# Kernel tuning notes

Measured on AMD Instinct MI355X. Metric: run time of the kernel, lower is better.

## Reference

```python
import jax, jax.numpy as jnp
import numpy as np

B, T, C, NH = 4, 2048, 1024, 16
HS = C // NH  # 64


def setup_inputs() -> dict:
    key = jax.random.key(0)
    ks = jax.random.split(key, 3)
    x = jax.random.normal(ks[0], (B, T, C), dtype=jnp.float32)
    w_attn = jax.random.normal(ks[1], (C, 3 * C), dtype=jnp.float32) * (1.0 / np.sqrt(C))
    b_attn = jnp.zeros((3 * C,), dtype=jnp.float32)
    w_proj = jax.random.normal(ks[2], (C, C), dtype=jnp.float32) * (1.0 / np.sqrt(C))
    b_proj = jnp.zeros((C,), dtype=jnp.float32)
    return {"x": x, "w_attn": w_attn, "b_attn": b_attn, "w_proj": w_proj, "b_proj": b_proj}


def reference(x, w_attn, b_attn, w_proj, b_proj):
    Bx, Tx, Cx = x.shape
    qkv = x @ w_attn + b_attn                      # (B,T,3C)
    q, k, v = jnp.split(qkv, 3, axis=2)
    # faithful to torch: view(B,T,hs,nh).transpose(1,3) -> (B,nh,hs,T)
    def to_heads(t):
        return jnp.transpose(t.reshape(Bx, Tx, HS, NH), (0, 3, 2, 1))
    q, k, v = to_heads(q), to_heads(k), to_heads(v)
    # att[b,h,i,j] = q_i . k_j / sqrt(hs)
    att = jnp.einsum('bhdi,bhdj->bhij', q, k) * (1.0 / np.sqrt(HS))
    # buffer is tril.T == upper-triangular; keep i<=j, mask i>j
    keep = jnp.triu(jnp.ones((Tx, Tx), dtype=bool))[None, None]
    att = jnp.where(keep, att, -jnp.inf)
    att = jax.nn.softmax(att, axis=-2)             # normalize over i
    y = jnp.einsum('bhdi,bhij->bhdj', v, att)      # (B,nh,hs,T)
    y = jnp.transpose(y, (0, 3, 2, 1)).reshape(Bx, Tx, Cx)
    return y @ w_proj + b_proj
```

## Files before the change

kernel.cpp:

```cpp
#include <hip/hip_runtime.h>
#include <stdint.h>


typedef __attribute__((ext_vector_type(8))) _Float16 f16x8;
typedef __attribute__((ext_vector_type(4))) _Float16 f16x4;
typedef __attribute__((ext_vector_type(2))) _Float16 h2;
typedef __attribute__((ext_vector_type(2))) __fp16   fp16x2_t;
typedef __attribute__((ext_vector_type(4))) float    f32x4;

#define NT_   8192
#define NC_   1024
#define N3C_  3072

__device__ __forceinline__ uint32_t pkrtz(float a, float b){
  union { fp16x2_t h; uint32_t u; } cv;
  cv.h = __builtin_amdgcn_cvt_pkrtz(a, b);
  return cv.u;
}

__global__ void k_cvt(const float* __restrict__ src, _Float16* __restrict__ dst, int n4){
  int idx = blockIdx.x*blockDim.x + threadIdx.x;
  int stride = gridDim.x*blockDim.x;
  for (int i = idx; i < n4; i += stride){
    float4 v = ((const float4*)src)[i];
    f16x4 o;
    o[0] = (_Float16)v.x; o[1] = (_Float16)v.y;
    o[2] = (_Float16)v.z; o[3] = (_Float16)v.w;
    ((f16x4*)dst)[i] = o;
  }
}

__global__ void k_wattn_t(const float* __restrict__ w, _Float16* __restrict__ wt){
  int t = threadIdx.x;
  int m0 = blockIdx.x*128, c0 = blockIdx.y*32;
  int mcol = m0 + t;
  int part = mcol >> 10, rr = mcol & 1023;
  int mp = part*1024 + (rr & 15)*64 + (rr >> 4);
  alignas(16) _Float16 buf[32];
  #pragma unroll
  for (int cc = 0; cc < 32; cc++)
    buf[cc] = (_Float16)w[(size_t)(c0+cc)*N3C_ + mcol];
  uint4* dst = (uint4*)(wt + (size_t)mp*NC_ + c0);
  const uint4* sb = (const uint4*)buf;
  dst[0]=sb[0]; dst[1]=sb[1]; dst[2]=sb[2]; dst[3]=sb[3];
}

__global__ void k_wproj_t(const float* __restrict__ w, _Float16* __restrict__ wt){
  int t = threadIdx.x;
  int o0 = blockIdx.x*128, cp0 = blockIdx.y*32;
  int o = o0 + t;
  alignas(16) _Float16 buf[32];
  #pragma unroll
  for (int i = 0; i < 32; i++){
    int cp = cp0 + i;
    int row = (cp & 63)*16 + (cp >> 6);
    buf[i] = (_Float16)w[(size_t)row*NC_ + o];
  }
  uint4* dst = (uint4*)(wt + (size_t)o*NC_ + cp0);
  const uint4* sb = (const uint4*)buf;
  dst[0]=sb[0]; dst[1]=sb[1]; dst[2]=sb[2]; dst[3]=sb[3];
}

__global__ void k_bias(const float* __restrict__ ba, float* __restrict__ bp){
  int i = blockIdx.x*blockDim.x + threadIdx.x;
  int part = i >> 10, rr = i & 1023, h = rr >> 6, d = rr & 63;
  bp[i] = ba[part*1024 + d*16 + h];
}

template<int OUT_HALF>
__global__ __launch_bounds__(256) void k_gemm(
    const _Float16* __restrict__ A, const _Float16* __restrict__ BT,
    const float* __restrict__ bias, void* __restrict__ outp,
    _Float16* __restrict__ VTout,
    int M, int N, int K)
{
  __shared__ _Float16 As[128][40];
  __shared__ _Float16 Bs[128][40];
  int tid = threadIdx.x;
  int wave = tid >> 6, lane = tid & 63;
  int wr = wave >> 1, wc = wave & 1;
  int g = lane >> 4, l15 = lane & 15;
  f32x4 acc[4][4] = {};
  const _Float16* Ag = A  + (size_t)blockIdx.y*128*K;
  const _Float16* Bg = BT + (size_t)blockIdx.x*128*K;
  int srow = tid >> 1, skoff = (tid & 1)*16;
  const _Float16* apt = Ag + (size_t)srow*K + skoff;
  const _Float16* bpt = Bg + (size_t)srow*K + skoff;
  uint4 ra0 = *(const uint4*)apt;
  uint4 ra1 = *(const uint4*)(apt + 8);
  uint4 rb0 = *(const uint4*)bpt;
  uint4 rb1 = *(const uint4*)(bpt + 8);
  for (int kt = 0; kt < K; kt += 32){
    __syncthreads();
    *(uint4*)&As[srow][skoff]     = ra0;
    *(uint4*)&As[srow][skoff + 8] = ra1;
    *(uint4*)&Bs[srow][skoff]     = rb0;
    *(uint4*)&Bs[srow][skoff + 8] = rb1;
    __syncthreads();
    if (kt + 32 < K){
      ra0 = *(const uint4*)(apt + kt + 32);
      ra1 = *(const uint4*)(apt + kt + 40);
      rb0 = *(const uint4*)(bpt + kt + 32);
      rb1 = *(const uint4*)(bpt + kt + 40);
    }
    f16x8 af[4], bf[4];
    #pragma unroll
    for (int mi = 0; mi < 4; mi++) af[mi] = *(const f16x8*)&As[wr*64 + mi*16 + l15][g*8];
    #pragma unroll
    for (int ni = 0; ni < 4; ni++) bf[ni] = *(const f16x8*)&Bs[wc*64 + ni*16 + l15][g*8];
    #pragma unroll
    for (int mi = 0; mi < 4; mi++)
      #pragma unroll
      for (int ni = 0; ni < 4; ni++)
        acc[mi][ni] = __builtin_amdgcn_mfma_f32_16x16x32_f16(af[mi], bf[ni], acc[mi][ni], 0, 0, 0);
  }
  int rowBase = blockIdx.y*128 + wr*64;
  int colBase = blockIdx.x*128 + wc*64;
  if (OUT_HALF && colBase >= 2048){
    int b = rowBase >> 11;
    int t0 = (rowBase & 2047);
    #pragma unroll
    for (int mi = 0; mi < 4; mi++){
      #pragma unroll
      for (int ni = 0; ni < 4; ni++){
        int col = colBase + ni*16 + l15;
        int cc = col - 2048;
        int h = cc >> 6, d = cc & 63;
        float bv = bias[col];
        _Float16* dst = VTout + (((size_t)(b*16 + h)*64 + d)*2048) + t0 + mi*16 + g*4;
        f16x4 o;
        #pragma unroll
        for (int r = 0; r < 4; r++) o[r] = (_Float16)(acc[mi][ni][r] + bv);
        *(f16x4*)dst = o;
      }
    }
    return;
  }
  #pragma unroll
  for (int mi = 0; mi < 4; mi++){
    #pragma unroll
    for (int ni = 0; ni < 4; ni++){
      int col = colBase + ni*16 + l15;
      float bv = bias[col];
      #pragma unroll
      for (int r = 0; r < 4; r++){
        int row = rowBase + mi*16 + g*4 + r;
        float v = acc[mi][ni][r] + bv;
        if (OUT_HALF) ((_Float16*)outp)[(size_t)row*N + col] = (_Float16)v;
        else          ((float*)outp)[(size_t)row*N + col] = v;
      }
    }
  }
}

__global__ __launch_bounds__(256) void k_attn(
    const _Float16* __restrict__ qkv, const _Float16* __restrict__ VTb,
    _Float16* __restrict__ Y)
{
  __shared__ _Float16 Ks[2][64][64];
  __shared__ _Float16 Vs[2][64][64];
  __shared__ uint32_t Ps[4][16][32];
  int bid = blockIdx.x;
  int bh = bid & 63;
  int j = bid >> 6;
  const int jts[4] = { j, 15-j, 16+j, 31-j };
  int maxjt = 31 - j;
  int b = bh >> 4, h = bh & 15;
  int tid = threadIdx.x, wave = tid >> 6, lane = tid & 63;
  int g = lane >> 4, l15 = lane & 15;
  uint32_t* Pw = &Ps[wave][0][0] + l15*32;
  int xm = (l15 & 7) << 2;
  int swR = (l15 & 7) << 4;
  const _Float16 QS = (_Float16)0.18033688f;
  const float OFF = 12.0f;

  int q0[4];
  f16x8 qf0[4], qf1[4];
  #pragma unroll
  for (int t = 0; t < 4; t++){
    q0[t] = jts[t]*64 + wave*16;
    const _Float16* qp = qkv + (size_t)(b*2048 + q0[t] + l15)*N3C_ + 1024 + h*64;
    qf0[t] = *(const f16x8*)&qp[g*8] * QS;
    qf1[t] = *(const f16x8*)&qp[32 + g*8] * QS;
  }
  float lrun[4] = {0.f, 0.f, 0.f, 0.f};
  f32x4 acc[4][4] = {};

  int srow = tid >> 2;
  int sbyte = (tid & 3)*32;
  int swW = (srow & 7) << 4;
  const _Float16* kbase = qkv + (size_t)(b*2048 + srow)*N3C_ + h*64 + (sbyte>>1);
  const _Float16* vbase = VTb + ((size_t)bh*64 + srow)*2048 + (sbyte>>1);

  auto stage = [&](int buf, const uint4& k0, const uint4& k1,
                   const uint4& v0, const uint4& v1){
    char* kw = (char*)&Ks[buf][0][0] + srow*128;
    char* vw = (char*)&Vs[buf][0][0] + srow*128;
    *(uint4*)(kw + ( sbyte       ^ swW)) = k0;
    *(uint4*)(kw + ((sbyte + 16) ^ swW)) = k1;
    *(uint4*)(vw + ( sbyte       ^ swW)) = v0;
    *(uint4*)(vw + ((sbyte + 16) ^ swW)) = v1;
  };

  auto process = [&](const f16x8& qa, const f16x8& qb, float& lr,
                     f32x4* ac, int qt0, int i0, bool diag, int cur){
    const char* kb = (const char*)&Ks[cur][0][0];
    const char* vb = (const char*)&Vs[cur][0][0];
    f32x4 s2[4];
    #pragma unroll
    for (int nb = 0; nb < 4; nb++){
      const char* krow = kb + (nb*16 + l15)*128;
      f16x8 kf0 = *(const f16x8*)(krow + (( g*16)      ^ swR));
      f16x8 kf1 = *(const f16x8*)(krow + ((64 + g*16)  ^ swR));
      f32x4 z = {};
      z = __builtin_amdgcn_mfma_f32_16x16x32_f16(kf0, qa, z, 0, 0, 0);
      z = __builtin_amdgcn_mfma_f32_16x16x32_f16(kf1, qb, z, 0, 0, 0);
      s2[nb] = z;
    }
    float p[16];
    #pragma unroll
    for (int nb = 0; nb < 4; nb++)
      #pragma unroll
      for (int r = 0; r < 4; r++)
        p[nb*4 + r] = s2[nb][r];
    if (diag){
      int qidx = qt0 + l15;
      #pragma unroll
      for (int nb = 0; nb < 4; nb++)
        #pragma unroll
        for (int r = 0; r < 4; r++){
          int kidx = i0 + nb*16 + g*4 + r;
          if (kidx > qidx) p[nb*4 + r] = -3e30f;
        }
    }
    uint32_t pk[8];
    #pragma unroll
    for (int i = 0; i < 8; i++){
      float e0 = __builtin_amdgcn_exp2f(p[2*i]     - OFF);
      float e1 = __builtin_amdgcn_exp2f(p[2*i + 1] - OFF);
      pk[i] = pkrtz(e0, e1);
    }
    #pragma unroll
    for (int nb = 0; nb < 4; nb++)
      #pragma unroll
      for (int r2 = 0; r2 < 2; r2++)
        Pw[(nb*8 + g*2 + r2) ^ xm] = pk[nb*2 + r2];
    #pragma unroll
    for (int ks = 0; ks < 2; ks++){
      f16x8 pb = *(const f16x8*)&Pw[(ks*16 + g*4) ^ xm];
      #pragma unroll
      for (int db = 0; db < 4; db++){
        const char* vrow = vb + (db*16 + l15)*128;
        f16x8 vv = *(const f16x8*)(vrow + ((ks*64 + g*16) ^ swR));
        ac[db] = __builtin_amdgcn_mfma_f32_16x16x32_f16(vv, pb, ac[db], 0, 0, 0);
      }
    }
    const h2 ones = { (_Float16)1.0f, (_Float16)1.0f };
    union { uint32_t u; h2 h; } cv;
    float rs0 = 0.f, rs1 = 0.f;
    #pragma unroll
    for (int i = 0; i < 4; i++){
      cv.u = pk[i];     rs0 = __builtin_amdgcn_fdot2(cv.h, ones, rs0, false);
      cv.u = pk[i + 4]; rs1 = __builtin_amdgcn_fdot2(cv.h, ones, rs1, false);
    }
    lr += rs0 + rs1;
  };

  uint4 ka0 = *(const uint4*)&kbase[0];
  uint4 ka1 = *(const uint4*)&kbase[8];
  uint4 va0 = *(const uint4*)&vbase[0];
  uint4 va1 = *(const uint4*)&vbase[8];
  stage(0, ka0, ka1, va0, va1);
  __syncthreads();
  for (int it = 0; it <= maxjt; ++it){
    int cur = it & 1;
    if (it < maxjt){
      size_t ko = (size_t)(it+1)*64*N3C_;
      int    vo = (it+1)*64;
      ka0 = *(const uint4*)&kbase[ko];
      ka1 = *(const uint4*)&kbase[ko + 8];
      va0 = *(const uint4*)&vbase[vo];
      va1 = *(const uint4*)&vbase[vo + 8];
    }
    #pragma unroll
    for (int t = 0; t < 4; t++)
      if (it <= jts[t])
        process(qf0[t], qf1[t], lrun[t], acc[t], q0[t], it*64, it == jts[t], cur);
    if (it < maxjt) stage(cur ^ 1, ka0, ka1, va0, va1);
    __syncthreads();
  }

  #pragma unroll
  for (int t = 0; t < 4; t++){
    float rs = lrun[t];
    rs += __shfl_xor(rs, 16);
    rs += __shfl_xor(rs, 32);
    float inv = 1.0f / rs;
    _Float16* yb = Y + (size_t)(b*2048 + q0[t] + l15)*NC_ + h*64 + g*4;
    #pragma unroll
    for (int db = 0; db < 4; db++){
      f16x4 o;
      #pragma unroll
      for (int r = 0; r < 4; r++) o[r] = (_Float16)(acc[t][db][r]*inv);
      *(f16x4*)&yb[db*16] = o;
    }
  }
}

extern "C" void kernel_launch(void* const* d_in, const int* in_sizes, int n_in,
                              void* d_out, int out_size, void* d_ws, size_t ws_size,
                              hipStream_t stream)
{
  const float* x      = (const float*)d_in[0];
  const float* w_attn = (const float*)d_in[1];
  const float* b_attn = (const float*)d_in[2];
  const float* w_proj = (const float*)d_in[3];
  const float* b_proj = (const float*)d_in[4];
  float* out = (float*)d_out;
  char* ws = (char*)d_ws;
  _Float16* xb   = (_Float16*)(ws + 0);
  _Float16* wT   = (_Float16*)(ws + 16777216);
  _Float16* wpT  = (_Float16*)(ws + 23068672);
  float*    bp   = (float*)   (ws + 25165824);
  _Float16* qkv  = (_Float16*)(ws + 25178112);
  _Float16* VT   = (_Float16*)(ws + 75509760);
  _Float16* Y    = (_Float16*)(ws + 92286976);

  k_cvt<<<2048, 256, 0, stream>>>(x, xb, (NT_*NC_)/4);
  k_wattn_t<<<dim3(24, 32), 128, 0, stream>>>(w_attn, wT);
  k_wproj_t<<<dim3(8, 32), 128, 0, stream>>>(w_proj, wpT);
  k_bias<<<12, 256, 0, stream>>>(b_attn, bp);
  k_gemm<1><<<dim3(24, 64), 256, 0, stream>>>(xb, wT, bp, qkv, VT, NT_, N3C_, NC_);
  k_attn<<<512, 256, 0, stream>>>(qkv, VT, Y);
  k_gemm<0><<<dim3(8, 64), 256, 0, stream>>>(Y, wpT, b_proj, out, (_Float16*)nullptr, NT_, NC_, NC_);
}
```

Baseline: 197.5 us.

## Double GEMM K-tile and attention KV tile to cut barrier and staging overhead

The GEMM now stages 64-wide K slices per iteration instead of 32, with wider LDS rows and two MFMA sub-steps per tile. This halves the number of global-to-LDS round trips and barriers. The attention kernel processes 128 keys per iteration instead of 64, again halving loop iterations and syncs. In exchange, LDS use rises (about 80KB for attention), which can lower occupancy, and some diagonal tiles now compute a fully masked 64-key half.

```diff
diff --git a/kernel.cpp b/kernel.cpp
--- a/kernel.cpp
+++ b/kernel.cpp
@@ -74,8 +74,8 @@
     _Float16* __restrict__ VTout,
     int M, int N, int K)
 {
-  __shared__ _Float16 As[128][40];
-  __shared__ _Float16 Bs[128][40];
+  __shared__ _Float16 As[128][72];
+  __shared__ _Float16 Bs[128][72];
   int tid = threadIdx.x;
   int wave = tid >> 6, lane = tid & 63;
   int wr = wave >> 1, wc = wave & 1;
@@ -83,36 +83,43 @@
   f32x4 acc[4][4] = {};
   const _Float16* Ag = A  + (size_t)blockIdx.y*128*K;
   const _Float16* Bg = BT + (size_t)blockIdx.x*128*K;
-  int srow = tid >> 1, skoff = (tid & 1)*16;
+  int srow = tid >> 1, skoff = (tid & 1)*32;
   const _Float16* apt = Ag + (size_t)srow*K + skoff;
   const _Float16* bpt = Bg + (size_t)srow*K + skoff;
-  uint4 ra0 = *(const uint4*)apt;
-  uint4 ra1 = *(const uint4*)(apt + 8);
-  uint4 rb0 = *(const uint4*)bpt;
-  uint4 rb1 = *(const uint4*)(bpt + 8);
-  for (int kt = 0; kt < K; kt += 32){
+  uint4 ra[4], rb[4];
+  #pragma unroll
+  for (int i = 0; i < 4; i++){
+    ra[i] = *(const uint4*)(apt + i*8);
+    rb[i] = *(const uint4*)(bpt + i*8);
+  }
+  for (int kt = 0; kt < K; kt += 64){
     __syncthreads();
-    *(uint4*)&As[srow][skoff]     = ra0;
-    *(uint4*)&As[srow][skoff + 8] = ra1;
-    *(uint4*)&Bs[srow][skoff]     = rb0;
-    *(uint4*)&Bs[srow][skoff + 8] = rb1;
+    #pragma unroll
+    for (int i = 0; i < 4; i++){
+      *(uint4*)&As[srow][skoff + i*8] = ra[i];
+      *(uint4*)&Bs[srow][skoff + i*8] = rb[i];
+    }
     __syncthreads();
-    if (kt + 32 < K){
-      ra0 = *(const uint4*)(apt + kt + 32);
-      ra1 = *(const uint4*)(apt + kt + 40);
-      rb0 = *(const uint4*)(bpt + kt + 32);
-      rb1 = *(const uint4*)(bpt + kt + 40);
-    }
-    f16x8 af[4], bf[4];
-    #pragma unroll
-    for (int mi = 0; mi < 4; mi++) af[mi] = *(const f16x8*)&As[wr*64 + mi*16 + l15][g*8];
-    #pragma unroll
-    for (int ni = 0; ni < 4; ni++) bf[ni] = *(const f16x8*)&Bs[wc*64 + ni*16 + l15][g*8];
-    #pragma unroll
-    for (int mi = 0; mi < 4; mi++)
-      #pragma unroll
-      for (int ni = 0; ni < 4; ni++)
-        acc[mi][ni] = __builtin_amdgcn_mfma_f32_16x16x32_f16(af[mi], bf[ni], acc[mi][ni], 0, 0, 0);
+    if (kt + 64 < K){
+      #pragma unroll
+      for (int i = 0; i < 4; i++){
+        ra[i] = *(const uint4*)(apt + kt + 64 + i*8);
+        rb[i] = *(const uint4*)(bpt + kt + 64 + i*8);
+      }
+    }
+    #pragma unroll
+    for (int kk = 0; kk < 2; kk++){
+      f16x8 af[4], bf[4];
+      #pragma unroll
+      for (int mi = 0; mi < 4; mi++) af[mi] = *(const f16x8*)&As[wr*64 + mi*16 + l15][kk*32 + g*8];
+      #pragma unroll
+      for (int ni = 0; ni < 4; ni++) bf[ni] = *(const f16x8*)&Bs[wc*64 + ni*16 + l15][kk*32 + g*8];
+      #pragma unroll
+      for (int mi = 0; mi < 4; mi++)
+        #pragma unroll
+        for (int ni = 0; ni < 4; ni++)
+          acc[mi][ni] = __builtin_amdgcn_mfma_f32_16x16x32_f16(af[mi], bf[ni], acc[mi][ni], 0, 0, 0);
+    }
   }
   int rowBase = blockIdx.y*128 + wr*64;
   int colBase = blockIdx.x*128 + wc*64;
@@ -157,28 +164,28 @@
     const _Float16* __restrict__ qkv, const _Float16* __restrict__ VTb,
     _Float16* __restrict__ Y)
 {
-  __shared__ _Float16 Ks[2][64][64];
-  __shared__ _Float16 Vs[2][64][64];
-  __shared__ uint32_t Ps[4][16][32];
+  __shared__ _Float16 Ks[2][128][64];
+  __shared__ _Float16 Vs[2][64][128];
+  __shared__ uint32_t Ps[4][16][64];
   int bid = blockIdx.x;
   int bh = bid & 63;
   int j = bid >> 6;
   const int jts[4] = { j, 15-j, 16+j, 31-j };
-  int maxjt = 31 - j;
   int b = bh >> 4, h = bh & 15;
   int tid = threadIdx.x, wave = tid >> 6, lane = tid & 63;
   int g = lane >> 4, l15 = lane & 15;
-  uint32_t* Pw = &Ps[wave][0][0] + l15*32;
+  uint32_t* Pw = &Ps[wave][0][0] + l15*64;
   int xm = (l15 & 7) << 2;
   int swR = (l15 & 7) << 4;
   const _Float16 QS = (_Float16)0.18033688f;
   const float OFF = 12.0f;
 
-  int q0[4];
+  int q0[4], lastt[4];
   f16x8 qf0[4], qf1[4];
   #pragma unroll
   for (int t = 0; t < 4; t++){
     q0[t] = jts[t]*64 + wave*16;
+    lastt[t] = jts[t] >> 1;
     const _Float16* qp = qkv + (size_t)(b*2048 + q0[t] + l15)*N3C_ + 1024 + h*64;
     qf0[t] = *(const f16x8*)&qp[g*8] * QS;
     qf1[t] = *(const f16x8*)&qp[32 + g*8] * QS;
@@ -186,72 +193,70 @@
   float lrun[4] = {0.f, 0.f, 0.f, 0.f};
   f32x4 acc[4][4] = {};
 
-  int srow = tid >> 2;
-  int sbyte = (tid & 3)*32;
-  int swW = (srow & 7) << 4;
-  const _Float16* kbase = qkv + (size_t)(b*2048 + srow)*N3C_ + h*64 + (sbyte>>1);
-  const _Float16* vbase = VTb + ((size_t)bh*64 + srow)*2048 + (sbyte>>1);
-
-  auto stage = [&](int buf, const uint4& k0, const uint4& k1,
-                   const uint4& v0, const uint4& v1){
-    char* kw = (char*)&Ks[buf][0][0] + srow*128;
-    char* vw = (char*)&Vs[buf][0][0] + srow*128;
-    *(uint4*)(kw + ( sbyte       ^ swW)) = k0;
-    *(uint4*)(kw + ((sbyte + 16) ^ swW)) = k1;
-    *(uint4*)(vw + ( sbyte       ^ swW)) = v0;
-    *(uint4*)(vw + ((sbyte + 16) ^ swW)) = v1;
+  int krow = tid >> 1, kbyte = (tid & 1)*64;
+  int swK = (krow & 7) << 4;
+  int vrow = tid >> 2, vbyte = (tid & 3)*64;
+  int swV = (vrow & 7) << 4;
+  const _Float16* kbase = qkv + (size_t)(b*2048 + krow)*N3C_ + h*64 + (kbyte>>1);
+  const _Float16* vbase = VTb + ((size_t)bh*64 + vrow)*2048 + (vbyte>>1);
+
+  uint4 kr[4], vr[4];
+  auto loadkv = [&](int it){
+    const _Float16* kp = kbase + (size_t)it*128*N3C_;
+    const _Float16* vp = vbase + it*128;
+    #pragma unroll
+    for (int i = 0; i < 4; i++){
+      kr[i] = *(const uint4*)(kp + i*8);
+      vr[i] = *(const uint4*)(vp + i*8);
+    }
+  };
+  auto stage = [&](int buf){
+    char* kw = (char*)&Ks[buf][0][0] + krow*128;
+    char* vw = (char*)&Vs[buf][0][0] + vrow*256;
+    #pragma unroll
+    for (int i = 0; i < 4; i++){
+      *(uint4*)(kw + ((kbyte + i*16) ^ swK)) = kr[i];
+      *(uint4*)(vw + ((vbyte + i*16) ^ swV)) = vr[i];
+    }
   };
 
   auto process = [&](const f16x8& qa, const f16x8& qb, float& lr,
                      f32x4* ac, int qt0, int i0, bool diag, int cur){
     const char* kb = (const char*)&Ks[cur][0][0];
     const char* vb = (const char*)&Vs[cur][0][0];
-    f32x4 s2[4];
-    #pragma unroll
-    for (int nb = 0; nb < 4; nb++){
-      const char* krow = kb + (nb*16 + l15)*128;
-      f16x8 kf0 = *(const f16x8*)(krow + (( g*16)      ^ swR));
-      f16x8 kf1 = *(const f16x8*)(krow + ((64 + g*16)  ^ swR));
+    uint32_t pkv[16];
+    #pragma unroll
+    for (int nb = 0; nb < 8; nb++){
+      const char* krp = kb + (nb*16 + l15)*128;
+      f16x8 kf0 = *(const f16x8*)(krp + (( g*16)     ^ swR));
+      f16x8 kf1 = *(const f16x8*)(krp + ((64 + g*16) ^ swR));
       f32x4 z = {};
       z = __builtin_amdgcn_mfma_f32_16x16x32_f16(kf0, qa, z, 0, 0, 0);
       z = __builtin_amdgcn_mfma_f32_16x16x32_f16(kf1, qb, z, 0, 0, 0);
-      s2[nb] = z;
-    }
-    float p[16];
-    #pragma unroll
-    for (int nb = 0; nb < 4; nb++)
-      #pragma unroll
-      for (int r = 0; r < 4; r++)
-        p[nb*4 + r] = s2[nb][r];
-    if (diag){
-      int qidx = qt0 + l15;
-      #pragma unroll
-      for (int nb = 0; nb < 4; nb++)
-        #pragma unroll
-        for (int r = 0; r < 4; r++){
+      float e[4];
+      #pragma unroll
+      for (int r = 0; r < 4; r++){
+        float sv = z[r];
+        if (diag){
           int kidx = i0 + nb*16 + g*4 + r;
-          if (kidx > qidx) p[nb*4 + r] = -3e30f;
+          if (kidx > qt0 + l15) sv = -3e30f;
         }
-    }
-    uint32_t pk[8];
-    #pragma unroll
-    for (int i = 0; i < 8; i++){
-      float e0 = __builtin_amdgcn_exp2f(p[2*i]     - OFF);
-      float e1 = __builtin_amdgcn_exp2f(p[2*i + 1] - OFF);
-      pk[i] = pkrtz(e0, e1);
-    }
-    #pragma unroll
-    for (int nb = 0; nb < 4; nb++)
-      #pragma unroll
-      for (int r2 = 0; r2 < 2; r2++)
-        Pw[(nb*8 + g*2 + r2) ^ xm] = pk[nb*2 + r2];
-    #pragma unroll
-    for (int ks = 0; ks < 2; ks++){
+        e[r] = __builtin_amdgcn_exp2f(sv - OFF);
+      }
+      uint32_t p0 = pkrtz(e[0], e[1]);
+      uint32_t p1 = pkrtz(e[2], e[3]);
+      Pw[(nb*8 + g*2 + 0) ^ xm] = p0;
+      Pw[(nb*8 + g*2 + 1) ^ xm] = p1;
+      pkv[nb*2]     = p0;
+      pkv[nb*2 + 1] = p1;
+    }
+    #pragma unroll
+    for (int ks = 0; ks < 4; ks++){
       f16x8 pb = *(const f16x8*)&Pw[(ks*16 + g*4) ^ xm];
       #pragma unroll
       for (int db = 0; db < 4; db++){
-        const char* vrow = vb + (db*16 + l15)*128;
-        f16x8 vv = *(const f16x8*)(vrow + ((ks*64 + g*16) ^ swR));
+        const char* vrp = vb + (db*16 + l15)*256;
+        f16x8 vv = *(const f16x8*)(vrp + ((ks*64 + g*16) ^ swR));
         ac[db] = __builtin_amdgcn_mfma_f32_16x16x32_f16(vv, pb, ac[db], 0, 0, 0);
       }
     }
@@ -259,34 +264,25 @@
     union { uint32_t u; h2 h; } cv;
     float rs0 = 0.f, rs1 = 0.f;
     #pragma unroll
-    for (int i = 0; i < 4; i++){
-      cv.u = pk[i];     rs0 = __builtin_amdgcn_fdot2(cv.h, ones, rs0, false);
-      cv.u = pk[i + 4]; rs1 = __builtin_amdgcn_fdot2(cv.h, ones, rs1, false);
+    for (int i = 0; i < 8; i++){
+      cv.u = pkv[i];     rs0 = __builtin_amdgcn_fdot2(cv.h, ones, rs0, false);
+      cv.u = pkv[i + 8]; rs1 = __builtin_amdgcn_fdot2(cv.h, ones, rs1, false);
     }
     lr += rs0 + rs1;
   };
 
-  uint4 ka0 = *(const uint4*)&kbase[0];
-  uint4 ka1 = *(const uint4*)&kbase[8];
-  uint4 va0 = *(const uint4*)&vbase[0];
-  uint4 va1 = *(const uint4*)&vbase[8];
-  stage(0, ka0, ka1, va0, va1);
+  int nit = ((31 - j) >> 1) + 1;
+  loadkv(0);
+  stage(0);
   __syncthreads();
-  for (int it = 0; it <= maxjt; ++it){
+  for (int it = 0; it < nit; ++it){
     int cur = it & 1;
-    if (it < maxjt){
-      size_t ko = (size_t)(it+1)*64*N3C_;
-      int    vo = (it+1)*64;
-      ka0 = *(const uint4*)&kbase[ko];
-      ka1 = *(const uint4*)&kbase[ko + 8];
-      va0 = *(const uint4*)&vbase[vo];
-      va1 = *(const uint4*)&vbase[vo + 8];
-    }
+    if (it + 1 < nit) loadkv(it + 1);
     #pragma unroll
     for (int t = 0; t < 4; t++)
-      if (it <= jts[t])
-        process(qf0[t], qf1[t], lrun[t], acc[t], q0[t], it*64, it == jts[t], cur);
-    if (it < maxjt) stage(cur ^ 1, ka0, ka1, va0, va1);
+      if (it <= lastt[t])
+        process(qf0[t], qf1[t], lrun[t], acc[t], q0[t], it*128, it == lastt[t], cur);
+    if (it + 1 < nit) stage(cur ^ 1);
     __syncthreads();
   }
 
```

Measured after the change: 494.2 us. 150% more time.

## Load GEMM tiles directly into LDS and raise wave priority around attention MFMAs

Applied to the files above, without the earlier changes.

The GEMM stops staging A/B tiles through registers and instead issues gfx950 global_load_lds 16-byte transfers straight into shared memory. The LDS row padding is dropped so each wave's destination is contiguous. The register prefetch of the next k-tile is removed, so global loads are no longer overlapped with the MFMAs of the current tile, and the unpadded rows may cause bank conflicts on fragment reads. Separately, the attention kernel wraps its QK and PV MFMA blocks in s_setprio(1)/s_setprio(0) so waves in the matrix phase get scheduling priority over waves doing softmax or loads.

```diff
diff --git a/kernel.cpp b/kernel.cpp
--- a/kernel.cpp
+++ b/kernel.cpp
@@ -16,6 +16,10 @@
   union { fp16x2_t h; uint32_t u; } cv;
   cv.h = __builtin_amdgcn_cvt_pkrtz(a, b);
   return cv.u;
+}
+__device__ __forceinline__ void glds16(const _Float16* g, _Float16* l){
+  __builtin_amdgcn_global_load_lds((const __attribute__((address_space(1))) void*)g,
+                                   (__attribute__((address_space(3))) void*)l, 16, 0, 0);
 }
 
 __global__ void k_cvt(const float* __restrict__ src, _Float16* __restrict__ dst, int n4){
@@ -74,35 +78,28 @@
     _Float16* __restrict__ VTout,
     int M, int N, int K)
 {
-  __shared__ _Float16 As[128][40];
-  __shared__ _Float16 Bs[128][40];
+  __shared__ _Float16 As[128][32];
+  __shared__ _Float16 Bs[128][32];
   int tid = threadIdx.x;
   int wave = tid >> 6, lane = tid & 63;
   int wr = wave >> 1, wc = wave & 1;
   int g = lane >> 4, l15 = lane & 15;
   f32x4 acc[4][4] = {};
-  const _Float16* Ag = A  + (size_t)blockIdx.y*128*K;
-  const _Float16* Bg = BT + (size_t)blockIdx.x*128*K;
-  int srow = tid >> 1, skoff = (tid & 1)*16;
-  const _Float16* apt = Ag + (size_t)srow*K + skoff;
-  const _Float16* bpt = Bg + (size_t)srow*K + skoff;
-  uint4 ra0 = *(const uint4*)apt;
-  uint4 ra1 = *(const uint4*)(apt + 8);
-  uint4 rb0 = *(const uint4*)bpt;
-  uint4 rb1 = *(const uint4*)(bpt + 8);
+  int r0 = tid >> 2, cs = (tid & 3)*8;
+  const _Float16* a0 = A  + ((size_t)blockIdx.y*128 + r0)*K + cs;
+  const _Float16* b0 = BT + ((size_t)blockIdx.x*128 + r0)*K + cs;
+  _Float16* la0 = &As[r0][cs];
+  _Float16* la1 = &As[r0 + 64][cs];
+  _Float16* lb0 = &Bs[r0][cs];
+  _Float16* lb1 = &Bs[r0 + 64][cs];
+  size_t step64 = (size_t)64*K;
   for (int kt = 0; kt < K; kt += 32){
     __syncthreads();
-    *(uint4*)&As[srow][skoff]     = ra0;
-    *(uint4*)&As[srow][skoff + 8] = ra1;
-    *(uint4*)&Bs[srow][skoff]     = rb0;
-    *(uint4*)&Bs[srow][skoff + 8] = rb1;
+    glds16(a0 + kt,          la0);
+    glds16(a0 + kt + step64, la1);
+    glds16(b0 + kt,          lb0);
+    glds16(b0 + kt + step64, lb1);
     __syncthreads();
-    if (kt + 32 < K){
-      ra0 = *(const uint4*)(apt + kt + 32);
-      ra1 = *(const uint4*)(apt + kt + 40);
-      rb0 = *(const uint4*)(bpt + kt + 32);
-      rb1 = *(const uint4*)(bpt + kt + 40);
-    }
     f16x8 af[4], bf[4];
     #pragma unroll
     for (int mi = 0; mi < 4; mi++) af[mi] = *(const f16x8*)&As[wr*64 + mi*16 + l15][g*8];
@@ -207,6 +204,7 @@
     const char* kb = (const char*)&Ks[cur][0][0];
     const char* vb = (const char*)&Vs[cur][0][0];
     f32x4 s2[4];
+    __builtin_amdgcn_s_setprio(1);
     #pragma unroll
     for (int nb = 0; nb < 4; nb++){
       const char* krow = kb + (nb*16 + l15)*128;
@@ -217,6 +215,7 @@
       z = __builtin_amdgcn_mfma_f32_16x16x32_f16(kf1, qb, z, 0, 0, 0);
       s2[nb] = z;
     }
+    __builtin_amdgcn_s_setprio(0);
     float p[16];
     #pragma unroll
     for (int nb = 0; nb < 4; nb++)
@@ -245,6 +244,7 @@
       #pragma unroll
       for (int r2 = 0; r2 < 2; r2++)
         Pw[(nb*8 + g*2 + r2) ^ xm] = pk[nb*2 + r2];
+    __builtin_amdgcn_s_setprio(1);
     #pragma unroll
     for (int ks = 0; ks < 2; ks++){
       f16x8 pb = *(const f16x8*)&Pw[(ks*16 + g*4) ^ xm];
@@ -255,6 +255,7 @@
         ac[db] = __builtin_amdgcn_mfma_f32_16x16x32_f16(vv, pb, ac[db], 0, 0, 0);
       }
     }
+    __builtin_amdgcn_s_setprio(0);
     const h2 ones = { (_Float16)1.0f, (_Float16)1.0f };
     union { uint32_t u; h2 h; } cv;
     float rs0 = 0.f, rs1 = 0.f;
```

After: 203.3 us. 1.03x slower.
